# Kernel tuning notes

Hardware: AMD Instinct MI355X
Metric: run time of the kernel (lower is better)

Reference implementation:

```python
import jax, jax.numpy as jnp
import numpy as np

B, N, D, H, DM = 4, 1024, 1024, 16, 4096
DH = D // H
SCALE = DH ** -0.5
EPS = 1e-5


def layer_norm(x, g, b):
    mu = jnp.mean(x, axis=-1, keepdims=True)
    var = jnp.mean((x - mu) ** 2, axis=-1, keepdims=True)
    return (x - mu) * jax.lax.rsqrt(var + EPS) * g + b


def mha(q_in, k_in, v_in, Wq, bq, Wk, bk, Wv, bv, Wp, bp):
    # weights stored (in, out); torch Linear equivalent y = x @ W + b
    q = (q_in @ Wq + bq).reshape(B, -1, H, DH).transpose(0, 2, 1, 3)  # (B,H,Nq,DH)
    k = (k_in @ Wk + bk).reshape(B, -1, H, DH).transpose(0, 2, 1, 3)
    v = (v_in @ Wv + bv).reshape(B, -1, H, DH).transpose(0, 2, 1, 3)
    attn = jax.nn.softmax(jnp.einsum('bhqd,bhkd->bhqk', q, k) * SCALE, axis=-1)
    x = jnp.einsum('bhqk,bhkd->bhqd', attn, v).transpose(0, 2, 1, 3).reshape(B, -1, D)
    return x @ Wp + bp


def setup_inputs() -> dict:
    key = jax.random.key(0)
    ks = jax.random.split(key, 32)
    s = 0.02
    inp = {
        'tokens_enc': jax.random.normal(ks[0], (B, N, D), jnp.float32),
        'tokens_dec': jax.random.normal(ks[1], (B, N, D), jnp.float32),
        'PE_enc': jax.random.normal(ks[2], (B, N, D), jnp.float32),
        'PE_dec': jax.random.normal(ks[3], (B, N, D), jnp.float32),
    }
    names = ['sa_Wq', 'sa_Wk', 'sa_Wv', 'sa_Wp', 'ca_Wq', 'ca_Wk', 'ca_Wv', 'ca_Wp']
    for i, n in enumerate(names):
        inp[n] = jax.random.normal(ks[4 + i], (D, D), jnp.float32) * s
        inp[n.replace('W', 'b')] = jnp.zeros((D,), jnp.float32)
    inp['mlp_W1'] = jax.random.normal(ks[12], (D, DM), jnp.float32) * s
    inp['mlp_b1'] = jnp.zeros((DM,), jnp.float32)
    inp['mlp_W2'] = jax.random.normal(ks[13], (DM, D), jnp.float32) * s
    inp['mlp_b2'] = jnp.zeros((D,), jnp.float32)
    for i in (1, 2, 3):
        inp[f'ln{i}_g'] = jnp.ones((D,), jnp.float32)
        inp[f'ln{i}_b'] = jnp.zeros((D,), jnp.float32)
    return inp


def reference(tokens_enc, tokens_dec, PE_enc, PE_dec,
              sa_Wq, sa_bq, sa_Wk, sa_bk, sa_Wv, sa_bv, sa_Wp, sa_bp,
              ca_Wq, ca_bq, ca_Wk, ca_bk, ca_Wv, ca_bv, ca_Wp, ca_bp,
              mlp_W1, mlp_b1, mlp_W2, mlp_b2,
              ln1_g, ln1_b, ln2_g, ln2_b, ln3_g, ln3_b):
    # SA (pre-norm): q=k=ln(x)+PE_dec, v=ln(x)
    x2 = layer_norm(tokens_dec, ln1_g, ln1_b)
    qk = x2 + PE_dec
    tokens_dec = tokens_dec + mha(qk, qk, x2, sa_Wq, sa_bq, sa_Wk, sa_bk, sa_Wv, sa_bv, sa_Wp, sa_bp)
    # CA: q=ln(x)+PE_dec, k=enc+PE_enc, v=enc
    x2 = layer_norm(tokens_dec, ln2_g, ln2_b)
    tokens_dec = tokens_dec + mha(x2 + PE_dec, tokens_enc + PE_enc, tokens_enc,
                                  ca_Wq, ca_bq, ca_Wk, ca_bk, ca_Wv, ca_bv, ca_Wp, ca_bp)
    # FFD
    x2 = layer_norm(tokens_dec, ln3_g, ln3_b)
    h = jax.nn.gelu(x2 @ mlp_W1 + mlp_b1, approximate=False)
    return tokens_dec + (h @ mlp_W2 + mlp_b2)
```

## Files before the change

### kernel.cpp

```cpp
#include <hip/hip_runtime.h>
#include <hip/hip_bf16.h>
#include <math.h>

#define B_ 4
#define N_ 1024
#define D_ 1024
#define H_ 16
#define DH_ 64
#define DM_ 4096
#define NT_ (B_*N_)
#define EPS_ 1e-5f
#define SCALE_ 0.125f
#define CEXP_ 0.1803368801111244f

typedef unsigned short u16;
typedef short s16x8 __attribute__((ext_vector_type(8)));
typedef __bf16 y16x8 __attribute__((ext_vector_type(8)));
typedef float f32x4 __attribute__((ext_vector_type(4)));
typedef float f32x16 __attribute__((ext_vector_type(16)));

#define ZERO16 (f32x16){0.f,0.f,0.f,0.f,0.f,0.f,0.f,0.f,0.f,0.f,0.f,0.f,0.f,0.f,0.f,0.f}

__device__ __forceinline__ u16 f2bs(float f) {
  unsigned int u = __builtin_bit_cast(unsigned int, f);
  u += 0x7fffu + ((u >> 16) & 1u);
  return (u16)(u >> 16);
}

static __device__ __forceinline__ f32x4 MFMA(y16x8 a, y16x8 b, f32x4 c) {
  return __builtin_amdgcn_mfma_f32_16x16x32_bf16(a, b, c, 0, 0, 0);
}
static __device__ __forceinline__ f32x16 MFMA32(y16x8 a, y16x8 b, f32x16 c) {
  return __builtin_amdgcn_mfma_f32_32x32x16_bf16(a, b, c, 0, 0, 0);
}

static __device__ __forceinline__ unsigned cvtpk(float a, float b) {
  unsigned r;
  asm("v_cvt_pk_bf16_f32 %0, %1, %2" : "=v"(r) : "v"(a), "v"(b));
  return r;
}

static __device__ __forceinline__ void async16(void* lds, const void* g) {
  __builtin_amdgcn_global_load_lds(
      (const __attribute__((address_space(1))) unsigned int*)g,
      (__attribute__((address_space(3))) unsigned int*)lds, 16, 0, 0);
}

__global__ __launch_bounds__(256) void k_prep(
    const float* __restrict__ s0, const float* __restrict__ s1,
    const float* __restrict__ s2, const float* __restrict__ s3,
    const float* __restrict__ s4, const float* __restrict__ s5,
    const float* __restrict__ s6, const float* __restrict__ s7,
    u16* __restrict__ w8, const float* __restrict__ mW1,
    u16* __restrict__ w1T, const float* __restrict__ mW2,
    u16* __restrict__ w2T, const float* __restrict__ enc,
    const float* __restrict__ pe, u16* __restrict__ encpe,
    u16* __restrict__ encv) {
  __shared__ u16 tile[32][33];
  const int gid = blockIdx.x;
  const int t = threadIdx.x;
  if (gid < 16384) {
    const float* W;
    u16* Wt;
    int K, Ncols, n0, k0;
    if (gid < 8192) {
      int z = gid >> 10, rem = gid & 1023;
      W = z == 0 ? s0 : z == 1 ? s1 : z == 2 ? s2 : z == 3 ? s3
        : z == 4 ? s4 : z == 5 ? s5 : z == 6 ? s6 : s7;
      Wt = w8 + (size_t)z * D_ * D_;
      K = D_; Ncols = D_;
      n0 = (rem & 31) * 32; k0 = (rem >> 5) * 32;
    } else if (gid < 12288) {
      int rem = gid - 8192;
      W = mW1; Wt = w1T; K = D_; Ncols = DM_;
      n0 = (rem & 127) * 32; k0 = (rem >> 7) * 32;
    } else {
      int rem = gid - 12288;
      W = mW2; Wt = w2T; K = DM_; Ncols = D_;
      n0 = (rem & 31) * 32; k0 = (rem >> 5) * 32;
    }
    int tx = t & 31, ty = t >> 5;
#pragma unroll
    for (int i = 0; i < 4; ++i) {
      int k = k0 + ty + i * 8;
      tile[ty + i * 8][tx] = f2bs(W[(size_t)k * Ncols + n0 + tx]);
    }
    __syncthreads();
#pragma unroll
    for (int i = 0; i < 4; ++i) {
      int n = n0 + ty + i * 8;
      Wt[(size_t)n * K + k0 + tx] = tile[tx][ty + i * 8];
    }
  } else {
    int i = (gid - 16384) * 256 + t;
    float4 e = ((const float4*)enc)[i];
    float4 p = ((const float4*)pe)[i];
    union { u16 u[4]; uint2 v; } a, b;
    a.u[0] = f2bs(e.x + p.x); a.u[1] = f2bs(e.y + p.y);
    a.u[2] = f2bs(e.z + p.z); a.u[3] = f2bs(e.w + p.w);
    b.u[0] = f2bs(e.x); b.u[1] = f2bs(e.y); b.u[2] = f2bs(e.z); b.u[3] = f2bs(e.w);
    ((uint2*)encpe)[i] = a.v;
    ((uint2*)encv)[i] = b.v;
  }
}

__global__ __launch_bounds__(256) void k_ln(const float* __restrict__ x,
                                            const float* __restrict__ g,
                                            const float* __restrict__ bta,
                                            const float* __restrict__ pe,
                                            u16* __restrict__ x2o,
                                            u16* __restrict__ qko) {
  int row = blockIdx.x;
  int t = threadIdx.x;
  float4 v = ((const float4*)(x + (size_t)row * D_))[t];
  float s = v.x + v.y + v.z + v.w;
#pragma unroll
  for (int o = 1; o < 64; o <<= 1) s += __shfl_xor(s, o, 64);
  __shared__ float red[8];
  if ((t & 63) == 0) red[t >> 6] = s;
  __syncthreads();
  float mean = (red[0] + red[1] + red[2] + red[3]) * (1.0f / D_);
  float dx = v.x - mean, dy = v.y - mean, dz = v.z - mean, dw = v.w - mean;
  float s2 = dx * dx + dy * dy + dz * dz + dw * dw;
#pragma unroll
  for (int o = 1; o < 64; o <<= 1) s2 += __shfl_xor(s2, o, 64);
  if ((t & 63) == 0) red[4 + (t >> 6)] = s2;
  __syncthreads();
  float var = (red[4] + red[5] + red[6] + red[7]) * (1.0f / D_);
  float rstd = rsqrtf(var + EPS_);
  float4 gv = ((const float4*)g)[t];
  float4 bv = ((const float4*)bta)[t];
  float y0 = dx * rstd * gv.x + bv.x;
  float y1 = dy * rstd * gv.y + bv.y;
  float y2 = dz * rstd * gv.z + bv.z;
  float y3 = dw * rstd * gv.w + bv.w;
  union { u16 u[4]; uint2 v2; } o1;
  o1.u[0] = f2bs(y0); o1.u[1] = f2bs(y1); o1.u[2] = f2bs(y2); o1.u[3] = f2bs(y3);
  ((uint2*)(x2o + (size_t)row * D_))[t] = o1.v2;
  if (pe) {
    float4 pv = ((const float4*)(pe + (size_t)row * D_))[t];
    union { u16 u[4]; uint2 v2; } o2;
    o2.u[0] = f2bs(y0 + pv.x); o2.u[1] = f2bs(y1 + pv.y);
    o2.u[2] = f2bs(y2 + pv.z); o2.u[3] = f2bs(y3 + pv.w);
    ((uint2*)(qko + (size_t)row * D_))[t] = o2.v2;
  }
}

template <int EPI, int BM>
__global__ __launch_bounds__(512) void k_gemm(const u16* __restrict__ A,
                                              const u16* __restrict__ Bt,
                                              const float* __restrict__ bias,
                                              const float* __restrict__ res,
                                              float* __restrict__ outf,
                                              u16* __restrict__ outb,
                                              int M, int Nn, int K, int ldo) {
  constexpr int BN = 128, BK = 64;
  constexpr int FM = BM / 32;
  __shared__ __align__(128) char smem[2][(BM + BN) * BK * 2];
  const int t = threadIdx.x;
  const int wave = t >> 6, lane = t & 63, lg = lane >> 4, lc = lane & 15;
  const int nwg = gridDim.x * gridDim.y;
  const int bid = blockIdx.y * gridDim.x + blockIdx.x;
  const int lb = (bid & 7) * (nwg >> 3) + (bid >> 3);
  const int bx = lb % gridDim.x, by = lb / gridDim.x;
  const int m0 = by * BM, n0 = bx * BN;
  const int wm = (wave >> 2) * (BM / 2), wn = (wave & 3) * 32;
  f32x4 acc[FM][2];
#pragma unroll
  for (int i = 0; i < FM; ++i)
#pragma unroll
    for (int j = 0; j < 2; ++j) acc[i][j] = (f32x4){0.f, 0.f, 0.f, 0.f};
  const char* Ag = (const char*)(A + (size_t)m0 * K);
  const char* Bg = (const char*)(Bt + (size_t)n0 * K);
  const int sr = t >> 3, sp = t & 7;

  auto stage = [&](int bufi, int kt) {
    char* sA = smem[bufi];
    char* sB = smem[bufi] + BM * BK * 2;
#pragma unroll
    for (int rr = 0; rr < BM / 64; ++rr) {
      int row = rr * 64 + sr;
      int c = sp ^ (row & 7);
      async16(sA + (size_t)row * 128 + sp * 16,
              Ag + ((size_t)row * K + kt + c * 8) * 2);
    }
#pragma unroll
    for (int rr = 0; rr < 2; ++rr) {
      int row = rr * 64 + sr;
      int c = sp ^ (row & 7);
      async16(sB + (size_t)row * 128 + sp * 16,
              Bg + ((size_t)row * K + kt + c * 8) * 2);
    }
  };
  auto compute = [&](int bufi) {
    const char* sA = smem[bufi];
    const char* sB = smem[bufi] + BM * BK * 2;
#pragma unroll
    for (int ks = 0; ks < 2; ++ks) {
      y16x8 af[FM], bfr[2];
#pragma unroll
      for (int fm = 0; fm < FM; ++fm) {
        int R = wm + fm * 16 + lc;
        int pc = (ks * 4 + lg) ^ (R & 7);
        af[fm] = *(const y16x8*)(sA + (size_t)R * 128 + pc * 16);
      }
#pragma unroll
      for (int fn = 0; fn < 2; ++fn) {
        int R = wn + fn * 16 + lc;
        int pc = (ks * 4 + lg) ^ (R & 7);
        bfr[fn] = *(const y16x8*)(sB + (size_t)R * 128 + pc * 16);
      }
#pragma unroll
      for (int fm = 0; fm < FM; ++fm)
#pragma unroll
        for (int fn = 0; fn < 2; ++fn)
          acc[fm][fn] = MFMA(af[fm], bfr[fn], acc[fm][fn]);
    }
  };

  stage(0, 0);
  __syncthreads();
  int cur = 0;
  for (int kt = BK; kt < K; kt += BK) {
    stage(cur ^ 1, kt);
    compute(cur);
    __syncthreads();
    cur ^= 1;
  }
  compute(cur);

#pragma unroll
  for (int fm = 0; fm < FM; ++fm)
#pragma unroll
    for (int fn = 0; fn < 2; ++fn)
#pragma unroll
      for (int j = 0; j < 4; ++j) {
        int row = m0 + wm + fm * 16 + lg * 4 + j;
        int col = n0 + wn + fn * 16 + lc;
        float vv = acc[fm][fn][j] + bias[col];
        size_t idx = (size_t)row * ldo + col;
        if constexpr (EPI == 0) {
          outb[idx] = f2bs(vv);
        } else if constexpr (EPI == 1) {
          outf[idx] = vv + res[idx];
        } else {
          float gx = 0.5f * vv * (1.0f + erff(vv * 0.70710678118f));
          outb[idx] = f2bs(gx);
        }
      }
}

__global__ __launch_bounds__(512) void k_gemmG(
    const u16* __restrict__ A0, const u16* __restrict__ A1,
    const u16* __restrict__ A2, const u16* __restrict__ A3,
    const u16* __restrict__ A4, const u16* __restrict__ W0,
    const u16* __restrict__ W1, const u16* __restrict__ W2,
    const u16* __restrict__ W3, const u16* __restrict__ W4,
    const float* __restrict__ b0, const float* __restrict__ b1,
    const float* __restrict__ b2, const float* __restrict__ b3,
    const float* __restrict__ b4, u16* __restrict__ qk1,
    u16* __restrict__ vt1, u16* __restrict__ qk2, u16* __restrict__ vt2) {
  constexpr int BM = 128, BN = 128, BK = 64, K = D_;
  __shared__ __align__(128) char smem[2][(BM + BN) * BK * 2];
  const int z = blockIdx.z;
  const u16* A = z == 0 ? A0 : z == 1 ? A1 : z == 2 ? A2 : z == 3 ? A3 : A4;
  const u16* Bt = z == 0 ? W0 : z == 1 ? W1 : z == 2 ? W2 : z == 3 ? W3 : W4;
  const float* bias = z == 0 ? b0 : z == 1 ? b1 : z == 2 ? b2 : z == 3 ? b3 : b4;
  const int t = threadIdx.x;
  const int wave = t >> 6, lane = t & 63, lg = lane >> 4, lc = lane & 15;
  const int nwg = gridDim.x * gridDim.y;
  const int bid = blockIdx.y * gridDim.x + blockIdx.x;
  const int lb = (bid & 7) * (nwg >> 3) + (bid >> 3);
  const int bx = lb % gridDim.x, by = lb / gridDim.x;
  const int m0 = by * BM, n0 = bx * BN;
  const int wm = (wave >> 2) * 64, wn = (wave & 3) * 32;
  f32x4 acc[4][2];
#pragma unroll
  for (int i = 0; i < 4; ++i)
#pragma unroll
    for (int j = 0; j < 2; ++j) acc[i][j] = (f32x4){0.f, 0.f, 0.f, 0.f};
  const char* Ag = (const char*)(A + (size_t)m0 * K);
  const char* Bg = (const char*)(Bt + (size_t)n0 * K);
  const int sr = t >> 3, sp = t & 7;

  auto stage = [&](int bufi, int kt) {
    char* sA = smem[bufi];
    char* sB = smem[bufi] + BM * BK * 2;
#pragma unroll
    for (int rr = 0; rr < 2; ++rr) {
      int row = rr * 64 + sr;
      int c = sp ^ (row & 7);
      async16(sA + (size_t)row * 128 + sp * 16,
              Ag + ((size_t)row * K + kt + c * 8) * 2);
      async16(sB + (size_t)row * 128 + sp * 16,
              Bg + ((size_t)row * K + kt + c * 8) * 2);
    }
  };
  auto compute = [&](int bufi) {
    const char* sA = smem[bufi];
    const char* sB = smem[bufi] + BM * BK * 2;
#pragma unroll
    for (int ks = 0; ks < 2; ++ks) {
      y16x8 af[4], bfr[2];
#pragma unroll
      for (int fm = 0; fm < 4; ++fm) {
        int R = wm + fm * 16 + lc;
        int pc = (ks * 4 + lg) ^ (R & 7);
        af[fm] = *(const y16x8*)(sA + (size_t)R * 128 + pc * 16);
      }
#pragma unroll
      for (int fn = 0; fn < 2; ++fn) {
        int R = wn + fn * 16 + lc;
        int pc = (ks * 4 + lg) ^ (R & 7);
        bfr[fn] = *(const y16x8*)(sB + (size_t)R * 128 + pc * 16);
      }
#pragma unroll
      for (int fm = 0; fm < 4; ++fm)
#pragma unroll
        for (int fn = 0; fn < 2; ++fn)
          acc[fm][fn] = MFMA(af[fm], bfr[fn], acc[fm][fn]);
    }
  };

  stage(0, 0);
  __syncthreads();
  int cur = 0;
  for (int kt = BK; kt < K; kt += BK) {
    stage(cur ^ 1, kt);
    compute(cur);
    __syncthreads();
    cur ^= 1;
  }
  compute(cur);

  const bool isV = (z == 2) || (z == 4);
  if (!isV) {
    u16* outqk = (z == 3) ? qk2 : qk1;
    const int coff = (z == 1 || z == 3) ? D_ : 0;
#pragma unroll
    for (int fm = 0; fm < 4; ++fm)
#pragma unroll
      for (int fn = 0; fn < 2; ++fn)
#pragma unroll
        for (int j = 0; j < 4; ++j) {
          int row = m0 + wm + fm * 16 + lg * 4 + j;
          int col = n0 + wn + fn * 16 + lc;
          outqk[(size_t)row * (2 * D_) + coff + col] =
              f2bs(acc[fm][fn][j] + bias[col]);
        }
  } else {
    u16* outvt = (z == 2) ? vt1 : vt2;
#pragma unroll
    for (int fm = 0; fm < 4; ++fm)
#pragma unroll
      for (int fn = 0; fn < 2; ++fn) {
        int row0 = m0 + wm + fm * 16 + lg * 4;
        int col = n0 + wn + fn * 16 + lc;
        int bb = row0 >> 10, nn = row0 & (N_ - 1);
        int h = col >> 6, dh = col & 63;
        float bcol = bias[col];
        union { u16 u[4]; uint2 v; } pk;
#pragma unroll
        for (int j = 0; j < 4; ++j) pk.u[j] = f2bs(acc[fm][fn][j] + bcol);
        *(uint2*)&outvt[(((size_t)bb * H_ + h) * DH_ + dh) * N_ + nn] = pk.v;
      }
  }
}

__global__ __launch_bounds__(256) void k_attn(const u16* __restrict__ q, int qs,
                                              const u16* __restrict__ k, int ks2,
                                              const u16* __restrict__ vt,
                                              u16* __restrict__ out) {
  __shared__ __align__(16) u16 Kl[128][64];
  __shared__ __align__(16) u16 Vl[64][128];
  __shared__ __align__(16) u16 Ol[4][32][72];
  const int lb = blockIdx.x;
  const int bh = (lb & 7) | ((lb >> 6) << 3);
  const int qb = (lb >> 3) & 7;
  const int b = bh >> 4, h = bh & 15;
  const int t = threadIdx.x, wave = t >> 6, lane = t & 63;
  const int ql = lane & 31, hi = lane >> 5;
  const int q0 = qb * 128 + wave * 32;
  const u16* qp = q + ((size_t)b * N_ + q0) * qs + h * DH_;
  const u16* kp = k + (size_t)b * N_ * ks2 + h * DH_;
  const u16* vp = vt + ((size_t)bh * DH_) * N_;

  y16x8 aq[4];
#pragma unroll
  for (int s = 0; s < 4; ++s)
    aq[s] = *(const y16x8*)(qp + (size_t)ql * qs + s * 16 + hi * 8);

  f32x16 o0 = ZERO16, o1 = ZERO16;
  float m_r = -1e30f, l_r = 0.f;

  const int kr = t >> 3, kc = t & 7;
  const int vr = t >> 4, vc = t & 15;
  s16x8 kreg[4], vreg[4];
#pragma unroll
  for (int rr = 0; rr < 4; ++rr) {
    kreg[rr] = *(const s16x8*)(kp + (size_t)(rr * 32 + kr) * ks2 + kc * 8);
    vreg[rr] = *(const s16x8*)(vp + (size_t)(rr * 16 + vr) * N_ + vc * 8);
  }

  for (int kt = 0; kt < N_; kt += 128) {
    __syncthreads();
#pragma unroll
    for (int rr = 0; rr < 4; ++rr) {
      int krow = rr * 32 + kr;
      *(s16x8*)&Kl[krow][(kc ^ (krow & 7)) * 8] = kreg[rr];
      int vrow = rr * 16 + vr;
      *(s16x8*)&Vl[vrow][(vc ^ (vrow & 15)) * 8] = vreg[rr];
    }
    __syncthreads();
    if (kt + 128 < N_) {
#pragma unroll
      for (int rr = 0; rr < 4; ++rr) {
        kreg[rr] = *(const s16x8*)(kp + (size_t)(kt + 128 + rr * 32 + kr) * ks2 + kc * 8);
        vreg[rr] = *(const s16x8*)(vp + (size_t)(rr * 16 + vr) * N_ + kt + 128 + vc * 8);
      }
    }

#pragma unroll
    for (int sub = 0; sub < 2; ++sub) {
      f32x16 st0 = ZERO16, st1 = ZERO16;
      __builtin_amdgcn_s_setprio(1);
#pragma unroll
      for (int s = 0; s < 4; ++s) {
        int pc0 = ((s * 2 + hi) ^ (ql & 7)) * 8;
        y16x8 ak0 = *(const y16x8*)&Kl[sub * 64 + ql][pc0];
        y16x8 ak1 = *(const y16x8*)&Kl[sub * 64 + 32 + ql][pc0];
        st0 = MFMA32(ak0, aq[s], st0);
        st1 = MFMA32(ak1, aq[s], st1);
      }
      __builtin_amdgcn_s_setprio(0);

      float mx = st0[0];
#pragma unroll
      for (int r = 1; r < 16; ++r) mx = fmaxf(mx, st0[r]);
#pragma unroll
      for (int r = 0; r < 16; ++r) mx = fmaxf(mx, st1[r]);
      mx = fmaxf(mx, __shfl_xor(mx, 32, 64));
      if (!__all(mx - m_r <= 32.f)) {
        float mn = fmaxf(m_r, mx);
        float corr = exp2f((m_r - mn) * CEXP_);
        l_r *= corr;
        o0 = o0 * corr;
        o1 = o1 * corr;
        m_r = mn;
      }
      float ps = 0.f;
#pragma unroll
      for (int r = 0; r < 16; ++r) {
        float e = exp2f((st0[r] - m_r) * CEXP_); st0[r] = e; ps += e;
      }
#pragma unroll
      for (int r = 0; r < 16; ++r) {
        float e = exp2f((st1[r] - m_r) * CEXP_); st1[r] = e; ps += e;
      }
      ps += __shfl_xor(ps, 32, 64);
      l_r += ps;

      __builtin_amdgcn_s_setprio(1);
#pragma unroll
      for (int ks = 0; ks < 4; ++ks) {
        unsigned A0, A1, B0, B1;
        if (ks < 2) {
          const int il = ks * 8;
          A0 = cvtpk(st0[il + 0], st0[il + 1]);
          A1 = cvtpk(st0[il + 2], st0[il + 3]);
          B0 = cvtpk(st0[il + 4], st0[il + 5]);
          B1 = cvtpk(st0[il + 6], st0[il + 7]);
        } else {
          const int il = (ks - 2) * 8;
          A0 = cvtpk(st1[il + 0], st1[il + 1]);
          A1 = cvtpk(st1[il + 2], st1[il + 3]);
          B0 = cvtpk(st1[il + 4], st1[il + 5]);
          B1 = cvtpk(st1[il + 6], st1[il + 7]);
        }
        asm("v_permlane32_swap_b32 %0, %1" : "+v"(A0), "+v"(B0));
        asm("v_permlane32_swap_b32 %0, %1" : "+v"(A1), "+v"(B1));
        union { unsigned w[4]; y16x8 v; } fr;
        fr.w[0] = A0; fr.w[1] = A1; fr.w[2] = B0; fr.w[3] = B1;
        int ch0 = (sub * 8 + ks * 2 + hi) ^ (ql & 15);
        int ch1 = (sub * 8 + ks * 2 + hi) ^ ((32 + ql) & 15);
        y16x8 bv0 = *(const y16x8*)&Vl[ql][ch0 * 8];
        y16x8 bv1 = *(const y16x8*)&Vl[32 + ql][ch1 * 8];
        o0 = MFMA32(bv0, fr.v, o0);
        o1 = MFMA32(bv1, fr.v, o1);
      }
      __builtin_amdgcn_s_setprio(0);
    }
  }

  float rl = 1.f / l_r;
#pragma unroll
  for (int rq = 0; rq < 4; ++rq)
#pragma unroll
    for (int e = 0; e < 4; e += 2) {
      *(unsigned*)&Ol[wave][ql][8 * rq + 4 * hi + e] =
          cvtpk(o0[rq * 4 + e] * rl, o0[rq * 4 + e + 1] * rl);
      *(unsigned*)&Ol[wave][ql][32 + 8 * rq + 4 * hi + e] =
          cvtpk(o1[rq * 4 + e] * rl, o1[rq * 4 + e + 1] * rl);
    }
#pragma unroll
  for (int pp = 0; pp < 4; ++pp) {
    int row = pp * 8 + (lane >> 3);
    s16x8 vv = *(const s16x8*)&Ol[wave][row][(lane & 7) * 8];
    *(s16x8*)(out + ((size_t)b * N_ + q0 + row) * D_ + h * DH_ + (lane & 7) * 8) = vv;
  }
}

extern "C" void kernel_launch(void* const* d_in, const int* in_sizes, int n_in,
                              void* d_out, int out_size, void* d_ws, size_t ws_size,
                              hipStream_t stream) {
  const float* tokens_enc = (const float*)d_in[0];
  const float* tokens_dec = (const float*)d_in[1];
  const float* PE_enc = (const float*)d_in[2];
  const float* PE_dec = (const float*)d_in[3];
  const float* sa_Wq = (const float*)d_in[4];  const float* sa_bq = (const float*)d_in[5];
  const float* sa_Wk = (const float*)d_in[6];  const float* sa_bk = (const float*)d_in[7];
  const float* sa_Wv = (const float*)d_in[8];  const float* sa_bv = (const float*)d_in[9];
  const float* sa_Wp = (const float*)d_in[10]; const float* sa_bp = (const float*)d_in[11];
  const float* ca_Wq = (const float*)d_in[12]; const float* ca_bq = (const float*)d_in[13];
  const float* ca_Wk = (const float*)d_in[14]; const float* ca_bk = (const float*)d_in[15];
  const float* ca_Wv = (const float*)d_in[16]; const float* ca_bv = (const float*)d_in[17];
  const float* ca_Wp = (const float*)d_in[18]; const float* ca_bp = (const float*)d_in[19];
  const float* mlp_W1 = (const float*)d_in[20]; const float* mlp_b1 = (const float*)d_in[21];
  const float* mlp_W2 = (const float*)d_in[22]; const float* mlp_b2 = (const float*)d_in[23];
  const float* ln1_g = (const float*)d_in[24]; const float* ln1_b = (const float*)d_in[25];
  const float* ln2_g = (const float*)d_in[26]; const float* ln2_b = (const float*)d_in[27];
  const float* ln3_g = (const float*)d_in[28]; const float* ln3_b = (const float*)d_in[29];

  char* wsp = (char*)d_ws;
  size_t off = 0;
  auto alloc = [&](size_t bytes) -> char* {
    char* p = wsp + off;
    off += (bytes + 255) & ~(size_t)255;
    return p;
  };
  u16* w8   = (u16*)alloc((size_t)8 * D_ * D_ * 2);
  u16* w1T  = (u16*)alloc((size_t)DM_ * D_ * 2);
  u16* w2T  = (u16*)alloc((size_t)D_ * DM_ * 2);
  u16* encpe = (u16*)alloc((size_t)NT_ * D_ * 2);
  u16* encv  = (u16*)alloc((size_t)NT_ * D_ * 2);
  u16* x2b = (u16*)alloc((size_t)NT_ * D_ * 2);
  u16* qkb = (u16*)alloc((size_t)NT_ * D_ * 2);
  u16* qkm = (u16*)alloc((size_t)NT_ * 2 * D_ * 2);
  u16* qkm2 = (u16*)alloc((size_t)NT_ * 2 * D_ * 2);
  u16* vtb = (u16*)alloc((size_t)NT_ * D_ * 2);
  u16* vtb2 = (u16*)alloc((size_t)NT_ * D_ * 2);
  u16* attb = (u16*)alloc((size_t)NT_ * D_ * 2);
  float* dec1 = (float*)alloc((size_t)NT_ * D_ * 4);
  float* dec2 = (float*)alloc((size_t)NT_ * D_ * 4);
  u16* hb = (u16*)alloc((size_t)NT_ * DM_ * 2);

  const size_t DD = (size_t)D_ * D_;
  u16* wqT  = w8;
  u16* wkT  = w8 + 1 * DD;
  u16* wvT  = w8 + 2 * DD;
  u16* wpT  = w8 + 3 * DD;
  u16* cwqT = w8 + 4 * DD;
  u16* cwkT = w8 + 5 * DD;
  u16* cwvT = w8 + 6 * DD;
  u16* cwpT = w8 + 7 * DD;

  k_prep<<<dim3(20480), 256, 0, stream>>>(sa_Wq, sa_Wk, sa_Wv, sa_Wp,
                                          ca_Wq, ca_Wk, ca_Wv, ca_Wp, w8,
                                          mlp_W1, w1T, mlp_W2, w2T,
                                          tokens_enc, PE_enc, encpe, encv);

  k_ln<<<dim3(NT_), 256, 0, stream>>>(tokens_dec, ln1_g, ln1_b, PE_dec, x2b, qkb);
  k_gemmG<<<dim3(8, 32, 5), 512, 0, stream>>>(
      qkb, qkb, x2b, encpe, encv, wqT, wkT, wvT, cwkT, cwvT,
      sa_bq, sa_bk, sa_bv, ca_bk, ca_bv, qkm, vtb, qkm2, vtb2);
  k_attn<<<dim3(512), 256, 0, stream>>>(qkm, 2 * D_, qkm + D_, 2 * D_, vtb, attb);
  k_gemm<1, 64><<<dim3(8, 64), 512, 0, stream>>>(attb, wpT, sa_bp, tokens_dec,
                                                 dec1, nullptr, NT_, D_, D_, D_);

  k_ln<<<dim3(NT_), 256, 0, stream>>>(dec1, ln2_g, ln2_b, PE_dec, x2b, qkb);
  k_gemm<0, 64><<<dim3(8, 64), 512, 0, stream>>>(qkb, cwqT, ca_bq, nullptr,
                                                 nullptr, qkm2, NT_, D_, D_, 2 * D_);
  k_attn<<<dim3(512), 256, 0, stream>>>(qkm2, 2 * D_, qkm2 + D_, 2 * D_, vtb2, attb);
  k_gemm<1, 64><<<dim3(8, 64), 512, 0, stream>>>(attb, cwpT, ca_bp, dec1,
                                                 dec2, nullptr, NT_, D_, D_, D_);

  k_ln<<<dim3(NT_), 256, 0, stream>>>(dec2, ln3_g, ln3_b, nullptr, x2b, nullptr);
  k_gemm<2, 64><<<dim3(32, 64), 512, 0, stream>>>(x2b, w1T, mlp_b1, nullptr,
                                                  nullptr, hb, NT_, DM_, D_, DM_);
  k_gemm<1, 64><<<dim3(8, 64), 512, 0, stream>>>(hb, w2T, mlp_b2, dec2,
                                                 (float*)d_out, nullptr, NT_, D_, DM_, D_);
}
```

Measured before the change: 335.3 us.

## Split-K the MLP down-projection and enlarge the up-projection tile

The FC2 GEMM (K=4096) is split into two K halves that run as separate grid slices, each writing fp32 partials. A new reduction kernel then sums the partials and adds bias and residual. FC1 switches to a 128-row tile with half as many blocks. The split doubles the number of waves for the long-K GEMM to improve occupancy. In exchange it adds about 32MB of extra fp32 partial traffic plus an extra launch, and one partial buffer reuses the qkm allocation.

```diff
diff --git a/kernel.cpp b/kernel.cpp
--- a/kernel.cpp
+++ b/kernel.cpp
@@ -250,6 +250,117 @@
       }
 }
 
+__global__ __launch_bounds__(512) void k_gemmSK(const u16* __restrict__ A,
+                                                const u16* __restrict__ Bt,
+                                                float* __restrict__ p0,
+                                                float* __restrict__ p1,
+                                                int M, int Nn, int K, int kLen) {
+  constexpr int BM = 64, BN = 128, BK = 64;
+  __shared__ __align__(128) char smem[2][(BM + BN) * BK * 2];
+  const int t = threadIdx.x;
+  const int wave = t >> 6, lane = t & 63, lg = lane >> 4, lc = lane & 15;
+  const int nwg = gridDim.x * gridDim.y;
+  const int bid = blockIdx.y * gridDim.x + blockIdx.x;
+  const int lb = (bid & 7) * (nwg >> 3) + (bid >> 3);
+  const int bx = lb % gridDim.x, by = lb / gridDim.x;
+  const int m0 = by * BM, n0 = bx * BN;
+  const int z = blockIdx.z;
+  float* outf = z == 0 ? p0 : p1;
+  const int wm = (wave >> 2) * 32, wn = (wave & 3) * 32;
+  f32x4 acc[2][2];
+#pragma unroll
+  for (int i = 0; i < 2; ++i)
+#pragma unroll
+    for (int j = 0; j < 2; ++j) acc[i][j] = (f32x4){0.f, 0.f, 0.f, 0.f};
+  const char* Ag = (const char*)(A + (size_t)m0 * K + (size_t)z * kLen);
+  const char* Bg = (const char*)(Bt + (size_t)n0 * K + (size_t)z * kLen);
+  const int sr = t >> 3, sp = t & 7;
+
+  auto stage = [&](int bufi, int kt) {
+    char* sA = smem[bufi];
+    char* sB = smem[bufi] + BM * BK * 2;
+    {
+      int row = sr;
+      int c = sp ^ (row & 7);
+      async16(sA + (size_t)row * 128 + sp * 16,
+              Ag + ((size_t)row * K + kt + c * 8) * 2);
+    }
+#pragma unroll
+    for (int rr = 0; rr < 2; ++rr) {
+      int row = rr * 64 + sr;
+      int c = sp ^ (row & 7);
+      async16(sB + (size_t)row * 128 + sp * 16,
+              Bg + ((size_t)row * K + kt + c * 8) * 2);
+    }
+  };
+  auto compute = [&](int bufi) {
+    const char* sA = smem[bufi];
+    const char* sB = smem[bufi] + BM * BK * 2;
+#pragma unroll
+    for (int ks = 0; ks < 2; ++ks) {
+      y16x8 af[2], bfr[2];
+#pragma unroll
+      for (int fm = 0; fm < 2; ++fm) {
+        int R = wm + fm * 16 + lc;
+        int pc = (ks * 4 + lg) ^ (R & 7);
+        af[fm] = *(const y16x8*)(sA + (size_t)R * 128 + pc * 16);
+      }
+#pragma unroll
+      for (int fn = 0; fn < 2; ++fn) {
+        int R = wn + fn * 16 + lc;
+        int pc = (ks * 4 + lg) ^ (R & 7);
+        bfr[fn] = *(const y16x8*)(sB + (size_t)R * 128 + pc * 16);
+      }
+#pragma unroll
+      for (int fm = 0; fm < 2; ++fm)
+#pragma unroll
+        for (int fn = 0; fn < 2; ++fn)
+          acc[fm][fn] = MFMA(af[fm], bfr[fn], acc[fm][fn]);
+    }
+  };
+
+  stage(0, 0);
+  __syncthreads();
+  int cur = 0;
+  for (int kt = BK; kt < kLen; kt += BK) {
+    stage(cur ^ 1, kt);
+    compute(cur);
+    __syncthreads();
+    cur ^= 1;
+  }
+  compute(cur);
+
+#pragma unroll
+  for (int fm = 0; fm < 2; ++fm)
+#pragma unroll
+    for (int fn = 0; fn < 2; ++fn)
+#pragma unroll
+      for (int j = 0; j < 4; ++j) {
+        int row = m0 + wm + fm * 16 + lg * 4 + j;
+        int col = n0 + wn + fn * 16 + lc;
+        outf[(size_t)row * Nn + col] = acc[fm][fn][j];
+      }
+}
+
+__global__ __launch_bounds__(256) void k_red(const float* __restrict__ p0,
+                                             const float* __restrict__ p1,
+                                             const float* __restrict__ bias,
+                                             const float* __restrict__ res,
+                                             float* __restrict__ out) {
+  size_t i = (size_t)blockIdx.x * 256 + threadIdx.x;
+  int col4 = (int)(i & (D_ / 4 - 1));
+  float4 a = ((const float4*)p0)[i];
+  float4 c = ((const float4*)p1)[i];
+  float4 r = ((const float4*)res)[i];
+  float4 bb = ((const float4*)bias)[col4];
+  float4 o;
+  o.x = a.x + c.x + bb.x + r.x;
+  o.y = a.y + c.y + bb.y + r.y;
+  o.z = a.z + c.z + bb.z + r.z;
+  o.w = a.w + c.w + bb.w + r.w;
+  ((float4*)out)[i] = o;
+}
+
 __global__ __launch_bounds__(512) void k_gemmG(
     const u16* __restrict__ A0, const u16* __restrict__ A1,
     const u16* __restrict__ A2, const u16* __restrict__ A3,
@@ -553,6 +664,8 @@
   float* dec1 = (float*)alloc((size_t)NT_ * D_ * 4);
   float* dec2 = (float*)alloc((size_t)NT_ * D_ * 4);
   u16* hb = (u16*)alloc((size_t)NT_ * DM_ * 2);
+  float* p0 = (float*)alloc((size_t)NT_ * D_ * 4);
+  float* p1 = (float*)qkm;
 
   const size_t DD = (size_t)D_ * D_;
   u16* wqT  = w8;
@@ -585,8 +698,8 @@
                                                  dec2, nullptr, NT_, D_, D_, D_);
 
   k_ln<<<dim3(NT_), 256, 0, stream>>>(dec2, ln3_g, ln3_b, nullptr, x2b, nullptr);
-  k_gemm<2, 64><<<dim3(32, 64), 512, 0, stream>>>(x2b, w1T, mlp_b1, nullptr,
-                                                  nullptr, hb, NT_, DM_, D_, DM_);
-  k_gemm<1, 64><<<dim3(8, 64), 512, 0, stream>>>(hb, w2T, mlp_b2, dec2,
-                                                 (float*)d_out, nullptr, NT_, D_, DM_, D_);
-}
+  k_gemm<2, 128><<<dim3(32, 32), 512, 0, stream>>>(x2b, w1T, mlp_b1, nullptr,
+                                                   nullptr, hb, NT_, DM_, D_, DM_);
+  k_gemmSK<<<dim3(8, 64, 2), 512, 0, stream>>>(hb, w2T, p0, p1, NT_, D_, DM_, DM_ / 2);
+  k_red<<<dim3(NT_ * D_ / 1024), 256, 0, stream>>>(p0, p1, mlp_b2, dec2, (float*)d_out);
+}
```

New measurement: 344.2 us. 2.7% more time.
